# Optimization experiments

Measured on AMD Instinct MI355X. Metric: run time of the kernel, lower is better.

## Reference

```python
import jax, jax.numpy as jnp
import numpy as np

B, T, D, H = 4, 2048, 1024, 16
DH = D // H
T2 = T // 2
LN_EPS = 1e-5


def setup_inputs() -> dict:
    key = jax.random.key(0)
    ks = jax.random.split(key, 10)
    x = jax.random.normal(ks[0], (B, T, D), dtype=jnp.float32)
    query = jax.random.normal(ks[1], (1, 1, D), dtype=jnp.float32) * 0.02
    s = 1.0 / np.sqrt(D)
    Wk = jax.random.uniform(ks[2], (D, D), jnp.float32, -s, s)
    Wv = jax.random.uniform(ks[3], (D, D), jnp.float32, -s, s)
    Wt = jax.random.uniform(ks[4], (D, D // 2), jnp.float32, -s, s)
    bt = jax.random.uniform(ks[5], (D // 2,), jnp.float32, -s, s)
    Wm = jax.random.uniform(ks[6], (D, 1), jnp.float32, -s, s)
    bm = jax.random.uniform(ks[7], (1,), jnp.float32, -s, s)
    ln_g = jnp.ones((D,), jnp.float32)
    ln_b = jnp.zeros((D,), jnp.float32)
    return {"x": x, "query": query, "Wk": Wk, "Wv": Wv, "Wt": Wt,
            "bt": bt, "Wm": Wm, "bm": bm, "ln_g": ln_g, "ln_b": ln_b}


def reference(x, query, Wk, Wv, Wt, bt, Wm, bm, ln_g, ln_b):
    Bx, Tx, d = x.shape
    t2 = Tx // 2
    h, dh = H, DH
    # projections -> (B, T, H, dh)
    k = (x @ Wk).reshape(Bx, Tx, h, dh)
    v = (x @ Wv).reshape(Bx, Tx, h, dh)
    q = query.reshape(h, dh)  # single learned query, shared over all coarse positions
    # scores: (B, H, T) then broadcast to (B, H, T2, T) with position-dependent mask t > 2j
    scores = jnp.einsum('hd,bthd->bht', q, k) / jnp.sqrt(jnp.asarray(dh, x.dtype))
    j_idx = jnp.arange(t2)[:, None]   # (T2, 1)
    t_idx = jnp.arange(Tx)[None, :]   # (1, T)
    mask_bias = jnp.where(t_idx > 2 * j_idx, -jnp.inf, 0.0).astype(x.dtype)  # (T2, T)
    attn = jax.nn.softmax(scores[:, :, None, :] + mask_bias[None, None], axis=-1)  # (B,H,T2,T)
    pooled = jnp.einsum('bhjt,bthd->bjhd', attn, v).reshape(Bx, t2, d)  # (B, T2, d)
    # LayerNorm over last dim
    mu = jnp.mean(pooled, axis=-1, keepdims=True)
    var = jnp.mean(jnp.square(pooled - mu), axis=-1, keepdims=True)
    pooled_n = (pooled - mu) * jax.lax.rsqrt(var + LN_EPS) * ln_g + ln_b
    theta = pooled_n @ Wt + bt                 # (B, T2, d//2)
    mag = jax.nn.sigmoid(pooled_n @ Wm + bm)   # (B, T2, 1)
    return theta, mag
```

## Files before the change

kernel.cpp:

```cpp
#include <hip/hip_runtime.h>
#include <hip/hip_bf16.h>
#include <cstdint>
#include <cstddef>

constexpr int Bc  = 4;
constexpr int Tc  = 2048;
constexpr int Dc  = 1024;
constexpr int Hc  = 16;
constexpr int DHc = 64;
constexpr int T2c = 1024;
constexpr int NCc = 32;
constexpr int NEXT = 1152;
#define LN_EPS_F 1e-5f

typedef __attribute__((ext_vector_type(8))) short bf16x8;
typedef __attribute__((ext_vector_type(8))) ushort ushort8_t;
typedef __attribute__((ext_vector_type(4))) float f32x4;

__device__ inline ushort f2bf(float f) {
    union { float f; uint32_t u; } v; v.f = f;
    uint32_t r = v.u + 0x7FFFu + ((v.u >> 16) & 1u);
    return (ushort)(r >> 16);
}
__device__ inline float bf2f(ushort u) {
    union { uint32_t u; float f; } v; v.u = ((uint32_t)u) << 16;
    return v.f;
}

__device__ inline void async_copy16(const void* g, void* lds) {
    __builtin_amdgcn_global_load_lds(
        (const __attribute__((address_space(1))) void*)g,
        (__attribute__((address_space(3))) void*)lds, 16, 0, 0);
}

constexpr int PREP_CVT  = 8192;
constexpr int PREP_WV   = PREP_CVT + 1024;
constexpr int PREP_WT   = PREP_WV + 512;
constexpr int PREP_QK   = PREP_WT + 64;
constexpr int PREP_ZERO = PREP_QK + 56;

__global__ __launch_bounds__(256) void k_prep(const float* __restrict__ x,
                                              const float* __restrict__ Wv,
                                              const float* __restrict__ Wt,
                                              const float* __restrict__ Wk,
                                              const float* __restrict__ query,
                                              ushort* __restrict__ xb,
                                              ushort* __restrict__ WvXT,
                                              ushort* __restrict__ WtT) {
    __shared__ float tile[32][33];
    int blk = blockIdx.x;
    int tid = threadIdx.x;
    if (blk < PREP_CVT) {
        int i = (blk * 256 + tid) * 4;
        float4 f = *(const float4*)(x + i);
        ushort4 o;
        o.x = f2bf(f.x); o.y = f2bf(f.y); o.z = f2bf(f.z); o.w = f2bf(f.w);
        *(ushort4*)(xb + i) = o;
    } else if (blk < PREP_WV) {
        int b2 = blk - PREP_CVT;
        int bx = b2 & 31, by = b2 >> 5;
        int tx = tid & 31, ty = tid >> 5;
        #pragma unroll
        for (int r = 0; r < 32; r += 8)
            tile[ty + r][tx] = Wv[(size_t)(by * 32 + ty + r) * Dc + bx * 32 + tx];
        __syncthreads();
        #pragma unroll
        for (int r = 0; r < 32; r += 8)
            WvXT[(size_t)(bx * 32 + ty + r) * Dc + by * 32 + tx] = f2bf(tile[tx][ty + r]);
    } else if (blk < PREP_WT) {
        int b2 = blk - PREP_WV;
        int bx = b2 & 15, by = b2 >> 4;
        int tx = tid & 31, ty = tid >> 5;
        #pragma unroll
        for (int r = 0; r < 32; r += 8)
            tile[ty + r][tx] = Wt[(size_t)(by * 32 + ty + r) * (Dc / 2) + bx * 32 + tx];
        __syncthreads();
        #pragma unroll
        for (int r = 0; r < 32; r += 8)
            WtT[(size_t)(bx * 32 + ty + r) * Dc + by * 32 + tx] = f2bf(tile[tx][ty + r]);
    } else if (blk < PREP_QK) {
        int idx = (blk - PREP_WT) * 256 + tid;
        int h = idx >> 10, i = idx & (Dc - 1);
        const float* wrow = Wk + (size_t)i * Dc + h * DHc;
        const float* qh   = query + h * DHc;
        float s = 0.f;
        #pragma unroll 8
        for (int d = 0; d < DHc; ++d) s += wrow[d] * qh[d];
        WvXT[(size_t)(Dc + h) * Dc + i] = f2bf(s * 0.125f);
    } else {
        int idx = (blk - PREP_QK) * 256 + tid;
        uint4 z = {0, 0, 0, 0};
        *(uint4*)(WvXT + (size_t)1040 * Dc + idx * 8) = z;
    }
}

__global__ __launch_bounds__(256) void k_gemm_v(const ushort* __restrict__ A,
                                                const ushort* __restrict__ Bt,
                                                ushort* __restrict__ v,
                                                float* __restrict__ scores) {
    constexpr int K = Dc;
    __shared__ ushort As[128 * 64];
    __shared__ ushort Bs[64 * 64];
    int tid = threadIdx.x;
    int wid = tid >> 6, lane = tid & 63;
    int tile_m = blockIdx.x * 128, tile_n = blockIdx.y * 64;
    int wm = wid >> 1, wn = wid & 1;

    f32x4 acc[4][2] = {};

    int lrow = lane >> 3;
    int lchunk = lane & 7;
    int schunk = lchunk ^ lrow;
    int quad = lane >> 4, l15 = lane & 15;
    int sw = l15 & 7;

    for (int k0 = 0; k0 < K; k0 += 64) {
        #pragma unroll
        for (int r = 0; r < 4; ++r) {
            int rowgrp = wid * 4 + r;
            int row = rowgrp * 8 + lrow;
            async_copy16(A + (size_t)(tile_m + row) * K + k0 + schunk * 8,
                         &As[rowgrp * 8 * 64]);
        }
        #pragma unroll
        for (int r = 0; r < 2; ++r) {
            int rowgrp = wid * 2 + r;
            int row = rowgrp * 8 + lrow;
            async_copy16(Bt + (size_t)(tile_n + row) * K + k0 + schunk * 8,
                         &Bs[rowgrp * 8 * 64]);
        }
        __syncthreads();

        bf16x8 a_frag[4][2], b_frag[2][2];
        #pragma unroll
        for (int s = 0; s < 2; ++s) {
            int gc = s * 4 + quad;
            #pragma unroll
            for (int i = 0; i < 4; ++i)
                a_frag[i][s] = *(const bf16x8*)&As[(wm * 64 + i * 16 + l15) * 64 + ((gc ^ sw) * 8)];
            #pragma unroll
            for (int j = 0; j < 2; ++j)
                b_frag[j][s] = *(const bf16x8*)&Bs[(wn * 32 + j * 16 + l15) * 64 + ((gc ^ sw) * 8)];
        }
        #pragma unroll
        for (int s = 0; s < 2; ++s)
            #pragma unroll
            for (int i = 0; i < 4; ++i)
                #pragma unroll
                for (int j = 0; j < 2; ++j)
                    acc[i][j] = __builtin_amdgcn_mfma_f32_16x16x32_bf16(
                        a_frag[i][s], b_frag[j][s], acc[i][j], 0, 0, 0);
        __syncthreads();
    }

    #pragma unroll
    for (int j = 0; j < 2; ++j) {
        int col = tile_n + wn * 32 + j * 16 + l15;
        #pragma unroll
        for (int i = 0; i < 4; ++i) {
            #pragma unroll
            for (int r = 0; r < 4; ++r) {
                int row = tile_m + wm * 64 + i * 16 + quad * 4 + r;
                float val = acc[i][j][r];
                if (col < Dc) {
                    v[(size_t)row * Dc + col] = f2bf(val);
                } else if (col < Dc + Hc) {
                    int h = col - Dc;
                    int b2 = row >> 11, t = row & (Tc - 1);
                    scores[((size_t)b2 * Hc + h) * Tc + t] = val;
                }
            }
        }
    }
}

__global__ __launch_bounds__(256) void k_gemm_t(const ushort* __restrict__ A,
                                                const ushort* __restrict__ Bt,
                                                const float* __restrict__ bias,
                                                float* __restrict__ C,
                                                int N, int K) {
    __shared__ ushort As[128 * 64];
    __shared__ ushort Bs[64 * 64];
    int tid = threadIdx.x;
    int wid = tid >> 6, lane = tid & 63;
    int tile_m = blockIdx.x * 128, tile_n = blockIdx.y * 64;
    int wm = wid >> 1, wn = wid & 1;

    f32x4 acc[4][2] = {};

    int lrow = lane >> 3;
    int lchunk = lane & 7;
    int schunk = lchunk ^ lrow;
    int quad = lane >> 4, l15 = lane & 15;
    int sw = l15 & 7;

    for (int k0 = 0; k0 < K; k0 += 64) {
        #pragma unroll
        for (int r = 0; r < 4; ++r) {
            int rowgrp = wid * 4 + r;
            int row = rowgrp * 8 + lrow;
            async_copy16(A + (size_t)(tile_m + row) * K + k0 + schunk * 8,
                         &As[rowgrp * 8 * 64]);
        }
        #pragma unroll
        for (int r = 0; r < 2; ++r) {
            int rowgrp = wid * 2 + r;
            int row = rowgrp * 8 + lrow;
            async_copy16(Bt + (size_t)(tile_n + row) * K + k0 + schunk * 8,
                         &Bs[rowgrp * 8 * 64]);
        }
        __syncthreads();

        bf16x8 a_frag[4][2], b_frag[2][2];
        #pragma unroll
        for (int s = 0; s < 2; ++s) {
            int gc = s * 4 + quad;
            #pragma unroll
            for (int i = 0; i < 4; ++i)
                a_frag[i][s] = *(const bf16x8*)&As[(wm * 64 + i * 16 + l15) * 64 + ((gc ^ sw) * 8)];
            #pragma unroll
            for (int j = 0; j < 2; ++j)
                b_frag[j][s] = *(const bf16x8*)&Bs[(wn * 32 + j * 16 + l15) * 64 + ((gc ^ sw) * 8)];
        }
        #pragma unroll
        for (int s = 0; s < 2; ++s)
            #pragma unroll
            for (int i = 0; i < 4; ++i)
                #pragma unroll
                for (int j = 0; j < 2; ++j)
                    acc[i][j] = __builtin_amdgcn_mfma_f32_16x16x32_bf16(
                        a_frag[i][s], b_frag[j][s], acc[i][j], 0, 0, 0);
        __syncthreads();
    }

    #pragma unroll
    for (int j = 0; j < 2; ++j) {
        int col = tile_n + wn * 32 + j * 16 + l15;
        float bv = bias[col];
        #pragma unroll
        for (int i = 0; i < 4; ++i) {
            #pragma unroll
            for (int r = 0; r < 4; ++r) {
                int row = tile_m + wm * 64 + i * 16 + quad * 4 + r;
                C[(size_t)row * N + col] = acc[i][j][r] + bv;
            }
        }
    }
}

__global__ __launch_bounds__(64) void k_chunk(const float* __restrict__ scores,
                                              const ushort* __restrict__ v,
                                              float* __restrict__ chunkL,
                                              float* __restrict__ chunkAcc) {
    int idx = blockIdx.x;
    int c = idx & (NCc - 1);
    int bh = idx / NCc;
    int h = bh & (Hc - 1), b = bh / Hc;
    int lane = threadIdx.x;
    int tgrp = lane >> 3;
    int dgrp = lane & 7;
    int t0 = c * 64;
    const float* srow = scores + (size_t)bh * Tc + t0;
    const ushort* vbase = v + ((size_t)b * Tc + t0) * Dc + h * DHc + dgrp * 8;
    float acc[8] = {};
    float lsum = 0.f;
    #pragma unroll
    for (int it = 0; it < 8; ++it) {
        int t = it * 8 + tgrp;
        float e = expf(srow[t]);
        ushort8_t vv = *(const ushort8_t*)(vbase + (size_t)t * Dc);
        #pragma unroll
        for (int k = 0; k < 8; ++k) acc[k] += e * bf2f(vv[k]);
        lsum += e;
    }
    #pragma unroll
    for (int m = 8; m < 64; m <<= 1) {
        #pragma unroll
        for (int k = 0; k < 8; ++k) acc[k] += __shfl_xor(acc[k], m);
        lsum += __shfl_xor(lsum, m);
    }
    if (tgrp == 0) {
        float4 lo = {acc[0], acc[1], acc[2], acc[3]};
        float4 hi = {acc[4], acc[5], acc[6], acc[7]};
        *(float4*)&chunkAcc[(size_t)idx * DHc + dgrp * 8]     = lo;
        *(float4*)&chunkAcc[(size_t)idx * DHc + dgrp * 8 + 4] = hi;
        if (dgrp == 0) chunkL[idx] = lsum;
    }
}

__global__ __launch_bounds__(64) void k_emit(const float* __restrict__ scores,
                                             const ushort* __restrict__ v,
                                             const float* __restrict__ chunkL,
                                             const float* __restrict__ chunkAcc,
                                             ushort* __restrict__ pooled) {
    int idx = blockIdx.x;
    int c = idx & (NCc - 1);
    int bh = idx / NCc;
    int h = bh & (Hc - 1), b = bh / Hc;
    int lane = threadIdx.x;
    int tgrp = lane >> 3, dgrp = lane & 7;
    int t0 = c * 64;
    __shared__ float E[64];
    __shared__ ushort vs[64 * DHc];
    E[lane] = expf(scores[(size_t)bh * Tc + t0 + lane]);
    const ushort* vbase = v + ((size_t)b * Tc + t0) * Dc + h * DHc + dgrp * 8;
    #pragma unroll
    for (int it = 0; it < 8; ++it) {
        int t = it * 8 + tgrp;
        *(ushort8_t*)&vs[t * DHc + dgrp * 8] = *(const ushort8_t*)(vbase + (size_t)t * Dc);
    }
    float acc = 0.f;
    for (int cc = 0; cc < c; ++cc)
        acc += chunkAcc[((size_t)bh * NCc + cc) * DHc + lane];
    float lP = (lane < c) ? chunkL[bh * NCc + lane] : 0.f;
    #pragma unroll
    for (int m = 1; m < 64; m <<= 1) lP += __shfl_xor(lP, m);
    float l = lP;
    __syncthreads();
    #pragma unroll 4
    for (int t = 0; t < 64; t += 2) {
        float e = E[t];
        acc += e * bf2f(vs[t * DHc + lane]);
        l += e;
        int j = (t0 + t) >> 1;
        pooled[((size_t)b * T2c + j) * Dc + h * DHc + lane] = f2bf(acc / l);
        float e2 = E[t + 1];
        acc += e2 * bf2f(vs[(t + 1) * DHc + lane]);
        l += e2;
    }
}

__global__ __launch_bounds__(256) void k_lnmag(const ushort* __restrict__ pooled,
                                               const float* __restrict__ g,
                                               const float* __restrict__ be,
                                               const float* __restrict__ Wm,
                                               const float* __restrict__ bm,
                                               ushort* __restrict__ out,
                                               float* __restrict__ mag) {
    int row = blockIdx.x;
    const ushort* p = pooled + (size_t)row * Dc;
    int tid = threadIdx.x;
    __shared__ float red[256];
    __shared__ float mu_s, rstd_s;
    float x4[4];
    {
        ushort4 u = *(const ushort4*)(p + tid * 4);
        x4[0] = bf2f(u.x); x4[1] = bf2f(u.y); x4[2] = bf2f(u.z); x4[3] = bf2f(u.w);
    }
    red[tid] = x4[0] + x4[1] + x4[2] + x4[3];
    __syncthreads();
    for (int off = 128; off > 0; off >>= 1) {
        if (tid < off) red[tid] += red[tid + off];
        __syncthreads();
    }
    if (tid == 0) mu_s = red[0] * (1.f / Dc);
    __syncthreads();
    float mu = mu_s;
    float vs = 0.f;
    #pragma unroll
    for (int k = 0; k < 4; ++k) { float d = x4[k] - mu; vs += d * d; }
    red[tid] = vs;
    __syncthreads();
    for (int off = 128; off > 0; off >>= 1) {
        if (tid < off) red[tid] += red[tid + off];
        __syncthreads();
    }
    if (tid == 0) rstd_s = rsqrtf(red[0] * (1.f / Dc) + LN_EPS_F);
    __syncthreads();
    float rstd = rstd_s;
    int i = tid * 4;
    float4 gv = *(const float4*)(g + i);
    float4 bv = *(const float4*)(be + i);
    float4 wv = *(const float4*)(Wm + i);
    float n0 = (x4[0] - mu) * rstd * gv.x + bv.x;
    float n1 = (x4[1] - mu) * rstd * gv.y + bv.y;
    float n2 = (x4[2] - mu) * rstd * gv.z + bv.z;
    float n3 = (x4[3] - mu) * rstd * gv.w + bv.w;
    ushort4 o;
    o.x = f2bf(n0); o.y = f2bf(n1); o.z = f2bf(n2); o.w = f2bf(n3);
    *(ushort4*)(out + (size_t)row * Dc + i) = o;
    red[tid] = bf2f(o.x) * wv.x + bf2f(o.y) * wv.y + bf2f(o.z) * wv.z + bf2f(o.w) * wv.w;
    __syncthreads();
    for (int off = 128; off > 0; off >>= 1) {
        if (tid < off) red[tid] += red[tid + off];
        __syncthreads();
    }
    if (tid == 0) {
        float z = red[0] + bm[0];
        mag[row] = 1.f / (1.f + expf(-z));
    }
}

extern "C" void kernel_launch(void* const* d_in, const int* in_sizes, int n_in,
                              void* d_out, int out_size, void* d_ws, size_t ws_size,
                              hipStream_t stream) {
    const float* x     = (const float*)d_in[0];
    const float* query = (const float*)d_in[1];
    const float* Wk    = (const float*)d_in[2];
    const float* Wv    = (const float*)d_in[3];
    const float* Wt    = (const float*)d_in[4];
    const float* bt    = (const float*)d_in[5];
    const float* Wm    = (const float*)d_in[6];
    const float* bm    = (const float*)d_in[7];
    const float* ln_g  = (const float*)d_in[8];
    const float* ln_b  = (const float*)d_in[9];
    float* out = (float*)d_out;

    char* w = (char*)d_ws;
    auto alloc = [&](size_t bytes) { char* p = w; w += (bytes + 255) & ~(size_t)255; return p; };
    ushort* v        = (ushort*)alloc((size_t)Bc * Tc * Dc * 2);
    ushort* pooled   = (ushort*)alloc((size_t)Bc * T2c * Dc * 2);
    ushort* xb       = (ushort*)alloc((size_t)Bc * Tc * Dc * 2);
    ushort* pooledn  = (ushort*)alloc((size_t)Bc * T2c * Dc * 2);
    ushort* WvXT     = (ushort*)alloc((size_t)NEXT * Dc * 2);
    ushort* WtT      = (ushort*)alloc((size_t)(Dc / 2) * Dc * 2);
    float*  scores   = (float*) alloc((size_t)Bc * Hc * Tc * 4);
    float*  chunkL   = (float*) alloc((size_t)Bc * Hc * NCc * 4);
    float*  chunkAcc = (float*) alloc((size_t)Bc * Hc * NCc * DHc * 4);

    k_prep<<<PREP_ZERO, 256, 0, stream>>>(x, Wv, Wt, Wk, query, xb, WvXT, WtT);
    k_gemm_v<<<dim3((Bc * Tc) / 128, 17), 256, 0, stream>>>(xb, WvXT, v, scores);
    k_chunk<<<Bc * Hc * NCc, 64, 0, stream>>>(scores, v, chunkL, chunkAcc);
    k_emit<<<Bc * Hc * NCc, 64, 0, stream>>>(scores, v, chunkL, chunkAcc, pooled);
    k_lnmag<<<Bc * T2c, 256, 0, stream>>>(pooled, ln_g, ln_b, Wm, bm, pooledn,
                                          out + (size_t)Bc * T2c * (Dc / 2));
    k_gemm_t<<<dim3((Bc * T2c) / 128, (Dc / 2) / 64), 256, 0, stream>>>(
        pooledn, WtT, bt, out, Dc / 2, Dc);
}
```

Before: 180.2 us.

## Fold LayerNorm and mag projection into the theta GEMM epilogue

Removes the separate LayerNorm/mag kernel. The emit kernel now accumulates per-row sum and sum-of-squares with atomics. The GEMM runs on raw pooled values against gamma-scaled Wt, with an extra column for Wm, and applies the mean/rstd correction algebraically in the epilogue. This saves one full read and write pass over the pooled activations and a kernel launch. In exchange it adds atomics in the emit loop, a memset, and variance computed as E[x²]-mu², which is less numerically stable.

```diff
diff --git a/kernel.cpp b/kernel.cpp
--- a/kernel.cpp
+++ b/kernel.cpp
@@ -11,6 +11,7 @@
 constexpr int T2c = 1024;
 constexpr int NCc = 32;
 constexpr int NEXT = 1152;
+constexpr int NT2  = 576;
 #define LN_EPS_F 1e-5f
 
 typedef __attribute__((ext_vector_type(8))) short bf16x8;
@@ -38,16 +39,25 @@
 constexpr int PREP_WT   = PREP_WV + 512;
 constexpr int PREP_QK   = PREP_WT + 64;
 constexpr int PREP_ZERO = PREP_QK + 56;
+constexpr int PREP_WMX  = PREP_ZERO + 4;
+constexpr int PREP_ZT   = PREP_WMX + 32;
+constexpr int PREP_MCOL = PREP_ZT + 1;
 
 __global__ __launch_bounds__(256) void k_prep(const float* __restrict__ x,
                                               const float* __restrict__ Wv,
                                               const float* __restrict__ Wt,
                                               const float* __restrict__ Wk,
                                               const float* __restrict__ query,
+                                              const float* __restrict__ g,
+                                              const float* __restrict__ be,
+                                              const float* __restrict__ Wm,
                                               ushort* __restrict__ xb,
                                               ushort* __restrict__ WvXT,
-                                              ushort* __restrict__ WtT) {
+                                              ushort* __restrict__ WtXT,
+                                              float* __restrict__ u,
+                                              float* __restrict__ w) {
     __shared__ float tile[32][33];
+    __shared__ float red2[512];
     int blk = blockIdx.x;
     int tid = threadIdx.x;
     if (blk < PREP_CVT) {
@@ -77,7 +87,26 @@
         __syncthreads();
         #pragma unroll
         for (int r = 0; r < 32; r += 8)
-            WtT[(size_t)(bx * 32 + ty + r) * Dc + by * 32 + tx] = f2bf(tile[tx][ty + r]);
+            WtXT[(size_t)(bx * 32 + ty + r) * Dc + by * 32 + tx] =
+                f2bf(tile[tx][ty + r] * g[by * 32 + tx]);
+        float pu = 0.f, pw = 0.f;
+        #pragma unroll
+        for (int k = 0; k < 4; ++k) {
+            int il = ty * 4 + k;
+            float tv = tile[il][tx];
+            pu += g[by * 32 + il] * tv;
+            pw += be[by * 32 + il] * tv;
+        }
+        red2[ty * 32 + tx] = pu;
+        red2[256 + ty * 32 + tx] = pw;
+        __syncthreads();
+        if (tid < 32) {
+            float su = 0.f, sw = 0.f;
+            #pragma unroll
+            for (int q = 0; q < 8; ++q) { su += red2[q * 32 + tid]; sw += red2[256 + q * 32 + tid]; }
+            atomicAdd(&u[bx * 32 + tid], su);
+            atomicAdd(&w[bx * 32 + tid], sw);
+        }
     } else if (blk < PREP_QK) {
         int idx = (blk - PREP_WT) * 256 + tid;
         int h = idx >> 10, i = idx & (Dc - 1);
@@ -87,10 +116,32 @@
         #pragma unroll 8
         for (int d = 0; d < DHc; ++d) s += wrow[d] * qh[d];
         WvXT[(size_t)(Dc + h) * Dc + i] = f2bf(s * 0.125f);
-    } else {
+    } else if (blk < PREP_ZERO) {
         int idx = (blk - PREP_QK) * 256 + tid;
         uint4 z = {0, 0, 0, 0};
         *(uint4*)(WvXT + (size_t)1040 * Dc + idx * 8) = z;
+    } else if (blk < PREP_WMX) {
+        int idx = (blk - PREP_ZERO) * 256 + tid;
+        WtXT[(size_t)512 * Dc + idx] = f2bf(g[idx] * Wm[idx]);
+    } else if (blk < PREP_ZT) {
+        int idx = (blk - PREP_WMX) * 256 + tid;
+        if (idx < 63 * Dc / 8) {
+            uint4 z = {0, 0, 0, 0};
+            *(uint4*)(WtXT + (size_t)513 * Dc + idx * 8) = z;
+        }
+    } else {
+        int i = tid * 4;
+        float4 gv  = *(const float4*)(g + i);
+        float4 wmv = *(const float4*)(Wm + i);
+        float4 bev = *(const float4*)(be + i);
+        red2[tid]       = gv.x * wmv.x + gv.y * wmv.y + gv.z * wmv.z + gv.w * wmv.w;
+        red2[256 + tid] = bev.x * wmv.x + bev.y * wmv.y + bev.z * wmv.z + bev.w * wmv.w;
+        __syncthreads();
+        for (int off = 128; off > 0; off >>= 1) {
+            if (tid < off) { red2[tid] += red2[tid + off]; red2[256 + tid] += red2[256 + tid + off]; }
+            __syncthreads();
+        }
+        if (tid == 0) { u[512] = red2[0]; w[512] = red2[256]; }
     }
 }
 
@@ -176,9 +227,15 @@
 
 __global__ __launch_bounds__(256) void k_gemm_t(const ushort* __restrict__ A,
                                                 const ushort* __restrict__ Bt,
-                                                const float* __restrict__ bias,
-                                                float* __restrict__ C,
-                                                int N, int K) {
+                                                const float* __restrict__ u,
+                                                const float* __restrict__ w,
+                                                const float* __restrict__ bt,
+                                                const float* __restrict__ bm,
+                                                const float* __restrict__ rowsum,
+                                                const float* __restrict__ rowsumsq,
+                                                float* __restrict__ theta,
+                                                float* __restrict__ mag) {
+    constexpr int K = Dc;
     __shared__ ushort As[128 * 64];
     __shared__ ushort Bs[64 * 64];
     int tid = threadIdx.x;
@@ -236,13 +293,21 @@
     #pragma unroll
     for (int j = 0; j < 2; ++j) {
         int col = tile_n + wn * 32 + j * 16 + l15;
-        float bv = bias[col];
+        float uc = (col <= Dc / 2) ? u[col] : 0.f;
+        float wc = (col <= Dc / 2) ? w[col] : 0.f;
         #pragma unroll
         for (int i = 0; i < 4; ++i) {
             #pragma unroll
             for (int r = 0; r < 4; ++r) {
                 int row = tile_m + wm * 64 + i * 16 + quad * 4 + r;
-                C[(size_t)row * N + col] = acc[i][j][r] + bv;
+                float mu = rowsum[row] * (1.f / Dc);
+                float rstd = rsqrtf(rowsumsq[row] * (1.f / Dc) - mu * mu + LN_EPS_F);
+                float val = rstd * (acc[i][j][r] - mu * uc) + wc;
+                if (col < Dc / 2) {
+                    theta[(size_t)row * (Dc / 2) + col] = val + bt[col];
+                } else if (col == Dc / 2) {
+                    mag[row] = 1.f / (1.f + expf(-(val + bm[0])));
+                }
             }
         }
     }
@@ -292,7 +357,9 @@
                                              const ushort* __restrict__ v,
                                              const float* __restrict__ chunkL,
                                              const float* __restrict__ chunkAcc,
-                                             ushort* __restrict__ pooled) {
+                                             ushort* __restrict__ pooled,
+                                             float* __restrict__ rowsum,
+                                             float* __restrict__ rowsumsq) {
     int idx = blockIdx.x;
     int c = idx & (NCc - 1);
     int bh = idx / NCc;
@@ -323,71 +390,18 @@
         acc += e * bf2f(vs[t * DHc + lane]);
         l += e;
         int j = (t0 + t) >> 1;
-        pooled[((size_t)b * T2c + j) * Dc + h * DHc + lane] = f2bf(acc / l);
+        float val = acc / l;
+        pooled[((size_t)b * T2c + j) * Dc + h * DHc + lane] = f2bf(val);
+        float s1 = val, s2 = val * val;
+        #pragma unroll
+        for (int m = 1; m < 64; m <<= 1) { s1 += __shfl_xor(s1, m); s2 += __shfl_xor(s2, m); }
+        if (lane == 0) {
+            atomicAdd(&rowsum[b * T2c + j], s1);
+            atomicAdd(&rowsumsq[b * T2c + j], s2);
+        }
         float e2 = E[t + 1];
         acc += e2 * bf2f(vs[(t + 1) * DHc + lane]);
         l += e2;
-    }
-}
-
-__global__ __launch_bounds__(256) void k_lnmag(const ushort* __restrict__ pooled,
-                                               const float* __restrict__ g,
-                                               const float* __restrict__ be,
-                                               const float* __restrict__ Wm,
-                                               const float* __restrict__ bm,
-                                               ushort* __restrict__ out,
-                                               float* __restrict__ mag) {
-    int row = blockIdx.x;
-    const ushort* p = pooled + (size_t)row * Dc;
-    int tid = threadIdx.x;
-    __shared__ float red[256];
-    __shared__ float mu_s, rstd_s;
-    float x4[4];
-    {
-        ushort4 u = *(const ushort4*)(p + tid * 4);
-        x4[0] = bf2f(u.x); x4[1] = bf2f(u.y); x4[2] = bf2f(u.z); x4[3] = bf2f(u.w);
-    }
-    red[tid] = x4[0] + x4[1] + x4[2] + x4[3];
-    __syncthreads();
-    for (int off = 128; off > 0; off >>= 1) {
-        if (tid < off) red[tid] += red[tid + off];
-        __syncthreads();
-    }
-    if (tid == 0) mu_s = red[0] * (1.f / Dc);
-    __syncthreads();
-    float mu = mu_s;
-    float vs = 0.f;
-    #pragma unroll
-    for (int k = 0; k < 4; ++k) { float d = x4[k] - mu; vs += d * d; }
-    red[tid] = vs;
-    __syncthreads();
-    for (int off = 128; off > 0; off >>= 1) {
-        if (tid < off) red[tid] += red[tid + off];
-        __syncthreads();
-    }
-    if (tid == 0) rstd_s = rsqrtf(red[0] * (1.f / Dc) + LN_EPS_F);
-    __syncthreads();
-    float rstd = rstd_s;
-    int i = tid * 4;
-    float4 gv = *(const float4*)(g + i);
-    float4 bv = *(const float4*)(be + i);
-    float4 wv = *(const float4*)(Wm + i);
-    float n0 = (x4[0] - mu) * rstd * gv.x + bv.x;
-    float n1 = (x4[1] - mu) * rstd * gv.y + bv.y;
-    float n2 = (x4[2] - mu) * rstd * gv.z + bv.z;
-    float n3 = (x4[3] - mu) * rstd * gv.w + bv.w;
-    ushort4 o;
-    o.x = f2bf(n0); o.y = f2bf(n1); o.z = f2bf(n2); o.w = f2bf(n3);
-    *(ushort4*)(out + (size_t)row * Dc + i) = o;
-    red[tid] = bf2f(o.x) * wv.x + bf2f(o.y) * wv.y + bf2f(o.z) * wv.z + bf2f(o.w) * wv.w;
-    __syncthreads();
-    for (int off = 128; off > 0; off >>= 1) {
-        if (tid < off) red[tid] += red[tid + off];
-        __syncthreads();
-    }
-    if (tid == 0) {
-        float z = red[0] + bm[0];
-        mag[row] = 1.f / (1.f + expf(-z));
     }
 }
 
@@ -406,24 +420,30 @@
     const float* ln_b  = (const float*)d_in[9];
     float* out = (float*)d_out;
 
-    char* w = (char*)d_ws;
-    auto alloc = [&](size_t bytes) { char* p = w; w += (bytes + 255) & ~(size_t)255; return p; };
+    char* w0 = (char*)d_ws;
+    auto alloc = [&](size_t bytes) { char* p = w0; w0 += (bytes + 255) & ~(size_t)255; return p; };
     ushort* v        = (ushort*)alloc((size_t)Bc * Tc * Dc * 2);
     ushort* pooled   = (ushort*)alloc((size_t)Bc * T2c * Dc * 2);
     ushort* xb       = (ushort*)alloc((size_t)Bc * Tc * Dc * 2);
-    ushort* pooledn  = (ushort*)alloc((size_t)Bc * T2c * Dc * 2);
     ushort* WvXT     = (ushort*)alloc((size_t)NEXT * Dc * 2);
-    ushort* WtT      = (ushort*)alloc((size_t)(Dc / 2) * Dc * 2);
+    ushort* WtXT     = (ushort*)alloc((size_t)NT2 * Dc * 2);
     float*  scores   = (float*) alloc((size_t)Bc * Hc * Tc * 4);
     float*  chunkL   = (float*) alloc((size_t)Bc * Hc * NCc * 4);
     float*  chunkAcc = (float*) alloc((size_t)Bc * Hc * NCc * DHc * 4);
-
-    k_prep<<<PREP_ZERO, 256, 0, stream>>>(x, Wv, Wt, Wk, query, xb, WvXT, WtT);
+    float*  rowsum   = (float*) alloc((size_t)Bc * T2c * 4);
+    float*  rowsumsq = (float*) alloc((size_t)Bc * T2c * 4);
+    float*  ucol     = (float*) alloc(520 * 4);
+    float*  wcol     = (float*) alloc(520 * 4);
+    size_t zbytes = (size_t)((char*)(wcol + 520) - (char*)rowsum);
+
+    hipMemsetAsync(rowsum, 0, zbytes, stream);
+    k_prep<<<PREP_MCOL, 256, 0, stream>>>(x, Wv, Wt, Wk, query, ln_g, ln_b, Wm,
+                                          xb, WvXT, WtXT, ucol, wcol);
     k_gemm_v<<<dim3((Bc * Tc) / 128, 17), 256, 0, stream>>>(xb, WvXT, v, scores);
     k_chunk<<<Bc * Hc * NCc, 64, 0, stream>>>(scores, v, chunkL, chunkAcc);
-    k_emit<<<Bc * Hc * NCc, 64, 0, stream>>>(scores, v, chunkL, chunkAcc, pooled);
-    k_lnmag<<<Bc * T2c, 256, 0, stream>>>(pooled, ln_g, ln_b, Wm, bm, pooledn,
-                                          out + (size_t)Bc * T2c * (Dc / 2));
-    k_gemm_t<<<dim3((Bc * T2c) / 128, (Dc / 2) / 64), 256, 0, stream>>>(
-        pooledn, WtT, bt, out, Dc / 2, Dc);
-}
+    k_emit<<<Bc * Hc * NCc, 64, 0, stream>>>(scores, v, chunkL, chunkAcc, pooled,
+                                             rowsum, rowsumsq);
+    k_gemm_t<<<dim3((Bc * T2c) / 128, NT2 / 64), 256, 0, stream>>>(
+        pooled, WtXT, ucol, wcol, bt, bm, rowsum, rowsumsq,
+        out, out + (size_t)Bc * T2c * (Dc / 2));
+}
```

Measured after the change: 187.6 us. 4.1% more time.

## Fuse chunk and emit passes into single-pass scan with inter-block flag chaining

Applied to the files above, without the earlier changes.

Replaces the two-kernel chunked prefix sum (per-chunk partial sums, then emit) with one kernel. Each block computes its local running sums once, publishes the chunk totals with a release flag, waits on the earlier chunks' flags, then adds the prefix and writes pooled outputs. This drops one launch and the second read of v and scores. In exchange, blocks spin-wait on one another, which relies on earlier chunks being scheduled first, and each thread keeps 64 extra registers of per-position partials.

```diff
diff --git a/kernel.cpp b/kernel.cpp
--- a/kernel.cpp
+++ b/kernel.cpp
@@ -38,6 +38,7 @@
 constexpr int PREP_WT   = PREP_WV + 512;
 constexpr int PREP_QK   = PREP_WT + 64;
 constexpr int PREP_ZERO = PREP_QK + 56;
+constexpr int PREP_FLG  = PREP_ZERO + 8;
 
 __global__ __launch_bounds__(256) void k_prep(const float* __restrict__ x,
                                               const float* __restrict__ Wv,
@@ -46,7 +47,8 @@
                                               const float* __restrict__ query,
                                               ushort* __restrict__ xb,
                                               ushort* __restrict__ WvXT,
-                                              ushort* __restrict__ WtT) {
+                                              ushort* __restrict__ WtT,
+                                              unsigned* __restrict__ flags) {
     __shared__ float tile[32][33];
     int blk = blockIdx.x;
     int tid = threadIdx.x;
@@ -87,10 +89,13 @@
         #pragma unroll 8
         for (int d = 0; d < DHc; ++d) s += wrow[d] * qh[d];
         WvXT[(size_t)(Dc + h) * Dc + i] = f2bf(s * 0.125f);
-    } else {
+    } else if (blk < PREP_ZERO) {
         int idx = (blk - PREP_QK) * 256 + tid;
         uint4 z = {0, 0, 0, 0};
         *(uint4*)(WvXT + (size_t)1040 * Dc + idx * 8) = z;
+    } else {
+        int idx = (blk - PREP_ZERO) * 256 + tid;
+        if (idx < Bc * Hc * NCc) flags[idx] = 0u;
     }
 }
 
@@ -248,50 +253,11 @@
     }
 }
 
-__global__ __launch_bounds__(64) void k_chunk(const float* __restrict__ scores,
-                                              const ushort* __restrict__ v,
-                                              float* __restrict__ chunkL,
-                                              float* __restrict__ chunkAcc) {
-    int idx = blockIdx.x;
-    int c = idx & (NCc - 1);
-    int bh = idx / NCc;
-    int h = bh & (Hc - 1), b = bh / Hc;
-    int lane = threadIdx.x;
-    int tgrp = lane >> 3;
-    int dgrp = lane & 7;
-    int t0 = c * 64;
-    const float* srow = scores + (size_t)bh * Tc + t0;
-    const ushort* vbase = v + ((size_t)b * Tc + t0) * Dc + h * DHc + dgrp * 8;
-    float acc[8] = {};
-    float lsum = 0.f;
-    #pragma unroll
-    for (int it = 0; it < 8; ++it) {
-        int t = it * 8 + tgrp;
-        float e = expf(srow[t]);
-        ushort8_t vv = *(const ushort8_t*)(vbase + (size_t)t * Dc);
-        #pragma unroll
-        for (int k = 0; k < 8; ++k) acc[k] += e * bf2f(vv[k]);
-        lsum += e;
-    }
-    #pragma unroll
-    for (int m = 8; m < 64; m <<= 1) {
-        #pragma unroll
-        for (int k = 0; k < 8; ++k) acc[k] += __shfl_xor(acc[k], m);
-        lsum += __shfl_xor(lsum, m);
-    }
-    if (tgrp == 0) {
-        float4 lo = {acc[0], acc[1], acc[2], acc[3]};
-        float4 hi = {acc[4], acc[5], acc[6], acc[7]};
-        *(float4*)&chunkAcc[(size_t)idx * DHc + dgrp * 8]     = lo;
-        *(float4*)&chunkAcc[(size_t)idx * DHc + dgrp * 8 + 4] = hi;
-        if (dgrp == 0) chunkL[idx] = lsum;
-    }
-}
-
-__global__ __launch_bounds__(64) void k_emit(const float* __restrict__ scores,
+__global__ __launch_bounds__(64) void k_scan(const float* __restrict__ scores,
                                              const ushort* __restrict__ v,
-                                             const float* __restrict__ chunkL,
-                                             const float* __restrict__ chunkAcc,
+                                             float* __restrict__ chunkL,
+                                             float* __restrict__ chunkAcc,
+                                             unsigned* __restrict__ flags,
                                              ushort* __restrict__ pooled) {
     int idx = blockIdx.x;
     int c = idx & (NCc - 1);
@@ -309,25 +275,48 @@
         int t = it * 8 + tgrp;
         *(ushort8_t*)&vs[t * DHc + dgrp * 8] = *(const ushort8_t*)(vbase + (size_t)t * Dc);
     }
-    float acc = 0.f;
-    for (int cc = 0; cc < c; ++cc)
-        acc += chunkAcc[((size_t)bh * NCc + cc) * DHc + lane];
-    float lP = (lane < c) ? chunkL[bh * NCc + lane] : 0.f;
-    #pragma unroll
-    for (int m = 1; m < 64; m <<= 1) lP += __shfl_xor(lP, m);
-    float l = lP;
-    __syncthreads();
+    __syncthreads();
+
+    float la[32], ll[32];
+    float acc = 0.f, l = 0.f;
     #pragma unroll 4
     for (int t = 0; t < 64; t += 2) {
         float e = E[t];
         acc += e * bf2f(vs[t * DHc + lane]);
         l += e;
-        int j = (t0 + t) >> 1;
-        pooled[((size_t)b * T2c + j) * Dc + h * DHc + lane] = f2bf(acc / l);
+        la[t >> 1] = acc;
+        ll[t >> 1] = l;
         float e2 = E[t + 1];
         acc += e2 * bf2f(vs[(t + 1) * DHc + lane]);
         l += e2;
     }
+
+    chunkAcc[(size_t)idx * DHc + lane] = acc;
+    if (lane == 0) chunkL[idx] = l;
+    __threadfence();
+    if (lane == 0)
+        __hip_atomic_store(&flags[idx], 1u, __ATOMIC_RELEASE, __HIP_MEMORY_SCOPE_AGENT);
+
+    if (lane == 0) {
+        for (int cc = 0; cc < c; ++cc)
+            while (__hip_atomic_load(&flags[bh * NCc + cc], __ATOMIC_ACQUIRE,
+                                     __HIP_MEMORY_SCOPE_AGENT) == 0u)
+                __builtin_amdgcn_s_sleep(8);
+    }
+    __syncthreads();
+    __threadfence();
+    float pfx = 0.f;
+    for (int cc = 0; cc < c; ++cc)
+        pfx += chunkAcc[((size_t)bh * NCc + cc) * DHc + lane];
+    float lP = (lane < c) ? chunkL[bh * NCc + lane] : 0.f;
+    #pragma unroll
+    for (int m = 1; m < 64; m <<= 1) lP += __shfl_xor(lP, m);
+
+    int j0 = t0 >> 1;
+    #pragma unroll 4
+    for (int j = 0; j < 32; ++j)
+        pooled[((size_t)b * T2c + j0 + j) * Dc + h * DHc + lane] =
+            f2bf((pfx + la[j]) / (lP + ll[j]));
 }
 
 __global__ __launch_bounds__(256) void k_lnmag(const ushort* __restrict__ pooled,
@@ -406,22 +395,22 @@
     const float* ln_b  = (const float*)d_in[9];
     float* out = (float*)d_out;
 
-    char* w = (char*)d_ws;
-    auto alloc = [&](size_t bytes) { char* p = w; w += (bytes + 255) & ~(size_t)255; return p; };
-    ushort* v        = (ushort*)alloc((size_t)Bc * Tc * Dc * 2);
-    ushort* pooled   = (ushort*)alloc((size_t)Bc * T2c * Dc * 2);
-    ushort* xb       = (ushort*)alloc((size_t)Bc * Tc * Dc * 2);
-    ushort* pooledn  = (ushort*)alloc((size_t)Bc * T2c * Dc * 2);
-    ushort* WvXT     = (ushort*)alloc((size_t)NEXT * Dc * 2);
-    ushort* WtT      = (ushort*)alloc((size_t)(Dc / 2) * Dc * 2);
-    float*  scores   = (float*) alloc((size_t)Bc * Hc * Tc * 4);
-    float*  chunkL   = (float*) alloc((size_t)Bc * Hc * NCc * 4);
-    float*  chunkAcc = (float*) alloc((size_t)Bc * Hc * NCc * DHc * 4);
-
-    k_prep<<<PREP_ZERO, 256, 0, stream>>>(x, Wv, Wt, Wk, query, xb, WvXT, WtT);
+    char* w0 = (char*)d_ws;
+    auto alloc = [&](size_t bytes) { char* p = w0; w0 += (bytes + 255) & ~(size_t)255; return p; };
+    ushort*   v        = (ushort*)  alloc((size_t)Bc * Tc * Dc * 2);
+    ushort*   pooled   = (ushort*)  alloc((size_t)Bc * T2c * Dc * 2);
+    ushort*   xb       = (ushort*)  alloc((size_t)Bc * Tc * Dc * 2);
+    ushort*   pooledn  = (ushort*)  alloc((size_t)Bc * T2c * Dc * 2);
+    ushort*   WvXT     = (ushort*)  alloc((size_t)NEXT * Dc * 2);
+    ushort*   WtT      = (ushort*)  alloc((size_t)(Dc / 2) * Dc * 2);
+    float*    scores   = (float*)   alloc((size_t)Bc * Hc * Tc * 4);
+    float*    chunkL   = (float*)   alloc((size_t)Bc * Hc * NCc * 4);
+    float*    chunkAcc = (float*)   alloc((size_t)Bc * Hc * NCc * DHc * 4);
+    unsigned* flags    = (unsigned*)alloc((size_t)Bc * Hc * NCc * 4);
+
+    k_prep<<<PREP_FLG, 256, 0, stream>>>(x, Wv, Wt, Wk, query, xb, WvXT, WtT, flags);
     k_gemm_v<<<dim3((Bc * Tc) / 128, 17), 256, 0, stream>>>(xb, WvXT, v, scores);
-    k_chunk<<<Bc * Hc * NCc, 64, 0, stream>>>(scores, v, chunkL, chunkAcc);
-    k_emit<<<Bc * Hc * NCc, 64, 0, stream>>>(scores, v, chunkL, chunkAcc, pooled);
+    k_scan<<<Bc * Hc * NCc, 64, 0, stream>>>(scores, v, chunkL, chunkAcc, flags, pooled);
     k_lnmag<<<Bc * T2c, 256, 0, stream>>>(pooled, ln_g, ln_b, Wm, bm, pooledn,
                                           out + (size_t)Bc * T2c * (Dc / 2));
     k_gemm_t<<<dim3((Bc * T2c) / 128, (Dc / 2) / 64), 256, 0, stream>>>(
```

Measured after the change: 564.9 us. +213.5%, slower.
